# Performance work log

Hardware: AMD Instinct MI355X
Metric: run time of the kernel (lower is better)

The kernel has to match this reference:

```python
import jax, jax.numpy as jnp
import numpy as np

DIM = 384
HEADS = 8


def _dwconv3x3(x, w):
    # depthwise 3x3, groups = channels, padding=1 (SAME)
    return jax.lax.conv_general_dilated(
        x, w, window_strides=(1, 1), padding='SAME',
        feature_group_count=x.shape[1],
        dimension_numbers=('NCHW', 'OIHW', 'NCHW'))


def _conv1x1(x, w):
    return jax.lax.conv_general_dilated(
        x, w, window_strides=(1, 1), padding='SAME',
        dimension_numbers=('NCHW', 'OIHW', 'NCHW'))


def setup_inputs() -> dict:
    key = jax.random.key(0)
    ks = jax.random.split(key, 7)
    b, h, w = 2, 128, 128
    f = lambda k, s: jax.random.normal(k, s, dtype=jnp.float32)
    return {
        'k_fea': f(ks[0], (b, DIM, h, w)),
        'v_fea': f(ks[1], (b, DIM, h, w)),
        'q_fea': f(ks[2], (b, DIM, h, w)),
        'wq': f(ks[3], (DIM, 1, 3, 3)) * 0.1,
        'wk': f(ks[4], (DIM, 1, 3, 3)) * 0.1,
        'wv': f(ks[5], (DIM, 1, 3, 3)) * 0.1,
        'wproj': f(ks[6], (DIM, DIM, 1, 1)) * 0.05,
        'temperature': jnp.ones((HEADS, 1, 1), jnp.float32),
        'attn_w': jnp.full((4,), 0.2, jnp.float32),  # attn1..attn4 scalars
    }


def reference(k_fea, v_fea, q_fea, wq, wk, wv, wproj, temperature, attn_w):
    b, c, h, w = q_fea.shape
    q = _dwconv3x3(q_fea, wq)
    k = _dwconv3x3(k_fea, wk)
    v = _dwconv3x3(v_fea, wv)
    hw = h * w
    C = c // HEADS  # channels per head
    rs = lambda t: t.reshape(b, HEADS, C, hw)
    q, k, v = rs(q), rs(k), rs(v)
    # F.normalize(dim=-1): L2 normalize with eps clamp
    norm = lambda t: t / jnp.maximum(
        jnp.linalg.norm(t, axis=-1, keepdims=True), 1e-12)
    q, k = norm(q), norm(k)
    # channel-channel attention [b, heads, C, C]
    attn = jnp.einsum('bhcn,bhdn->bhcd', q, k) * temperature
    ar = jnp.arange(C)
    neg_inf = jnp.float32(-jnp.inf)
    ks_list = [C // 2, C * 2 // 3, C * 3 // 4, C * 4 // 5]
    out = jnp.zeros((b, HEADS, C, hw), attn.dtype)
    for i, topk in enumerate(ks_list):
        idx = jax.lax.top_k(attn, topk)[1]          # [b,h,C,topk]
        mask = (idx[..., None] == ar).any(axis=-2)  # [b,h,C,C] bool
        a = jax.nn.softmax(jnp.where(mask, attn, neg_inf), axis=-1)
        out = out + attn_w[i] * jnp.einsum('bhcd,bhdn->bhcn', a, v)
    out = out.reshape(b, c, h, w)
    return _conv1x1(out, wproj)
```

## Files before the change

kernel.cpp:

```cpp
#include <hip/hip_runtime.h>
#include <stdint.h>

#define NB 2
#define CH 384
#define NH 8
#define CPH 48
#define IMG 128
#define HW 16384

typedef float f32x4 __attribute__((ext_vector_type(4)));
typedef short bf16x8 __attribute__((ext_vector_type(8)));
typedef short short4v __attribute__((ext_vector_type(4)));

__device__ inline unsigned short f2bf(float f){
    unsigned u = __builtin_bit_cast(unsigned, f);
    u += 0x7FFFu + ((u >> 16) & 1u);
    return (unsigned short)(u >> 16);
}
__device__ inline float bf2f(unsigned short h){
    unsigned u = ((unsigned)h) << 16;
    return __builtin_bit_cast(float, u);
}

__global__ __launch_bounds__(256) void k_conv3(
    const float* __restrict__ qf, const float* __restrict__ kf,
    const float* __restrict__ vf,
    const float* __restrict__ wq, const float* __restrict__ wk,
    const float* __restrict__ wv,
    unsigned short* __restrict__ Qh, unsigned short* __restrict__ Ql,
    unsigned short* __restrict__ Kh, unsigned short* __restrict__ Kl,
    unsigned short* __restrict__ Vc, float* __restrict__ ssqg)
{
    const int p = blockIdx.x;
    const int tensor = p / 768;
    const int bc = p % 768;
    const int ch = bc % CH, b = bc / CH;

    const float* plane; const float* wp9;
    unsigned short *oh, *ol;
    if (tensor == 0) { plane = qf + (size_t)bc * HW; wp9 = wq + ch * 9;
                       oh = Qh + (size_t)bc * HW; ol = Ql + (size_t)bc * HW; }
    else if (tensor == 1) { plane = kf + (size_t)bc * HW; wp9 = wk + ch * 9;
                       oh = Kh + (size_t)bc * HW; ol = Kl + (size_t)bc * HW; }
    else             { plane = vf + (size_t)bc * HW; wp9 = wv + ch * 9;
                       oh = Vc + (size_t)bc * HW; ol = nullptr; }

    float w9[9];
#pragma unroll
    for (int i = 0; i < 9; ++i) w9[i] = wp9[i];

    const int t = threadIdx.x;
    const int wvid = t >> 6, lane = t & 63;
    const int rb = lane >> 5, cx = lane & 31;

    float ssqacc = 0.f;

    for (int pass = 0; pass < 16; ++pass) {
        const int y = wvid * 32 + pass * 2 + rb;
        float o0 = 0.f, o1 = 0.f, o2 = 0.f, o3 = 0.f;
#pragma unroll
        for (int dy = 0; dy < 3; ++dy) {
            const int yy = y + dy - 1;
            const float vm = (yy >= 0 && yy < IMG) ? 1.f : 0.f;
            const int yc = yy < 0 ? 0 : (yy > IMG - 1 ? IMG - 1 : yy);
            float4 r4 = *(const float4*)(plane + yc * IMG + 4 * cx);
            r4.x *= vm; r4.y *= vm; r4.z *= vm; r4.w *= vm;
            float lf = __shfl(r4.w, (lane + 63) & 63);
            if (cx == 0) lf = 0.f;
            float rt = __shfl(r4.x, (lane + 1) & 63);
            if (cx == 31) rt = 0.f;
            const float a0 = w9[dy * 3], a1 = w9[dy * 3 + 1], a2 = w9[dy * 3 + 2];
            o0 += a0 * lf   + a1 * r4.x + a2 * r4.y;
            o1 += a0 * r4.x + a1 * r4.y + a2 * r4.z;
            o2 += a0 * r4.y + a1 * r4.z + a2 * r4.w;
            o3 += a0 * r4.z + a1 * r4.w + a2 * rt;
        }
        const int xb = 4 * cx;
        if (tensor < 2) {
            ssqacc += o0 * o0 + o1 * o1 + o2 * o2 + o3 * o3;
            unsigned short h0 = f2bf(o0), h1 = f2bf(o1), h2 = f2bf(o2), h3 = f2bf(o3);
            short4v hv = {(short)h0, (short)h1, (short)h2, (short)h3};
            short4v lv = {(short)f2bf(o0 - bf2f(h0)), (short)f2bf(o1 - bf2f(h1)),
                          (short)f2bf(o2 - bf2f(h2)), (short)f2bf(o3 - bf2f(h3))};
            *(short4v*)(oh + y * IMG + xb) = hv;
            *(short4v*)(ol + y * IMG + xb) = lv;
        } else {
            short4v pv = {(short)f2bf(o0), (short)f2bf(o1), (short)f2bf(o2), (short)f2bf(o3)};
            *(short4v*)(oh + y * IMG + xb) = pv;
        }
    }

    if (tensor < 2) {
#pragma unroll
        for (int off = 32; off; off >>= 1) ssqacc += __shfl_xor(ssqacc, off);
        __shared__ float ssr[4];
        if (lane == 0) ssr[wvid] = ssqacc;
        __syncthreads();
        if (t == 0) {
            int h = ch / CPH, c = ch % CPH;
            ssqg[(b * NH + h) * 96 + tensor * 48 + c] = ssr[0] + ssr[1] + ssr[2] + ssr[3];
        }
    }
}

__global__ __launch_bounds__(256) void k_gram2(
    const unsigned short* __restrict__ Qh, const unsigned short* __restrict__ Ql,
    const unsigned short* __restrict__ Kh, const unsigned short* __restrict__ Kl,
    float* __restrict__ Sg)
{
    __shared__ float sred[4][2304];
    const int t = threadIdx.x;
    const int s = blockIdx.x, bh = blockIdx.y;
    const int wid = t >> 6, lane = t & 63, quad = lane >> 4, l15 = lane & 15;
    const size_t pbase = (size_t)((bh >> 3) * CH + (bh & 7) * CPH) * HW;

    f32x4 acc[3][3];
#pragma unroll
    for (int i = 0; i < 3; ++i)
#pragma unroll
        for (int j = 0; j < 3; ++j) acc[i][j] = (f32x4){0.f, 0.f, 0.f, 0.f};

    const int k0 = s * 512 + wid * 128;
#pragma unroll
    for (int ks = 0; ks < 4; ++ks) {
        const int px = k0 + ks * 32 + quad * 8;
        bf16x8 qh[3], ql_[3], kh[3], kl[3];
#pragma unroll
        for (int i = 0; i < 3; ++i) {
            size_t off = pbase + (size_t)(i * 16 + l15) * HW + px;
            qh[i]  = *(const bf16x8*)(Qh + off);
            ql_[i] = *(const bf16x8*)(Ql + off);
            kh[i]  = *(const bf16x8*)(Kh + off);
            kl[i]  = *(const bf16x8*)(Kl + off);
        }
#pragma unroll
        for (int ci = 0; ci < 3; ++ci)
#pragma unroll
            for (int di = 0; di < 3; ++di) {
                acc[ci][di] = __builtin_amdgcn_mfma_f32_16x16x32_bf16(qh[ci],  kh[di], acc[ci][di], 0, 0, 0);
                acc[ci][di] = __builtin_amdgcn_mfma_f32_16x16x32_bf16(qh[ci],  kl[di], acc[ci][di], 0, 0, 0);
                acc[ci][di] = __builtin_amdgcn_mfma_f32_16x16x32_bf16(ql_[ci], kh[di], acc[ci][di], 0, 0, 0);
            }
    }
#pragma unroll
    for (int ci = 0; ci < 3; ++ci)
#pragma unroll
        for (int di = 0; di < 3; ++di)
#pragma unroll
            for (int r = 0; r < 4; ++r)
                sred[wid][(ci * 16 + quad * 4 + r) * 48 + di * 16 + l15] = acc[ci][di][r];
    __syncthreads();
    float* Sbh = Sg + (size_t)bh * 2304;
#pragma unroll
    for (int i = 0; i < 9; ++i) {
        int e = t * 9 + i;
        atomicAdd(&Sbh[e], sred[0][e] + sred[1][e] + sred[2][e] + sred[3][e]);
    }
}

__global__ void k_attn(const float* __restrict__ Sg, const float* __restrict__ ssqg,
                       const float* __restrict__ temp, const float* __restrict__ aw,
                       float* __restrict__ Mg)
{
    const int t = threadIdx.x;
    const int r = blockIdx.x * 4 + (t >> 6);
    const int lane = t & 63;
    const int c = r % 48, h = (r / 48) % NH, b = r / (48 * NH);
    const float* Srow = Sg + ((size_t)(b * NH + h) * 48 + c) * 48;
    const float* sq = ssqg + (size_t)(b * NH + h) * 96;

    float v = -3.0e38f;
    if (lane < 48) {
        float nq = fmaxf(sqrtf(sq[c]), 1e-12f);
        float nk = fmaxf(sqrtf(sq[48 + lane]), 1e-12f);
        v = Srow[lane] / (nq * nk) * temp[h];
    }
    float m = v;
#pragma unroll
    for (int off = 32; off; off >>= 1) m = fmaxf(m, __shfl_xor(m, off));
    int rank = 0;
    for (int e = 0; e < 48; ++e) {
        float ve = __shfl(v, e);
        rank += ((ve > v) || (ve == v && e < lane)) ? 1 : 0;
    }
    float ed = (lane < 48) ? __expf(v - m) : 0.f;
    const int K4[4] = {24, 32, 36, 38};
    float f = 0.f;
#pragma unroll
    for (int i = 0; i < 4; ++i) {
        float x = (rank < K4[i]) ? ed : 0.f;
#pragma unroll
        for (int off = 32; off; off >>= 1) x += __shfl_xor(x, off);
        if (rank < K4[i]) f += aw[i] / x;
    }
    if (lane < 48) Mg[((size_t)(b * NH + h) * 48 + c) * 48 + lane] = ed * f;
}

__global__ void k_w2(const float* __restrict__ wproj, const float* __restrict__ Mg,
                     unsigned short* __restrict__ W2)
{
    int idx = blockIdx.x * 256 + threadIdx.x;
    int gd = idx % 384; int co = (idx / 384) % 384; int b = idx / (384 * 384);
    int h = gd / 48, d = gd % 48;
    const float* wp = wproj + (size_t)co * 384 + h * 48;
    const float* Mp = Mg + (size_t)(b * NH + h) * 2304 + d;
    float s = 0.f;
#pragma unroll
    for (int cc = 0; cc < 48; ++cc) s += wp[cc] * Mp[cc * 48];
    W2[idx] = f2bf(s);
}

__global__ __launch_bounds__(256) void k_trans(const unsigned short* __restrict__ Vc,
                                               unsigned short* __restrict__ Vct)
{
    __shared__ unsigned short S[64][66];
    const int nt = blockIdx.x, ct = blockIdx.y, b = blockIdx.z;
    const int t = threadIdx.x, r = t >> 2, seg = t & 3;
    const unsigned short* src = Vc + (size_t)(b * CH + ct * 64 + r) * HW + nt * 64 + seg * 16;
    *(bf16x8*)&S[r][seg * 16]     = *(const bf16x8*)src;
    *(bf16x8*)&S[r][seg * 16 + 8] = *(const bf16x8*)(src + 8);
    __syncthreads();
    unsigned short tmp[16];
#pragma unroll
    for (int i = 0; i < 16; ++i) tmp[i] = S[seg * 16 + i][r];
    unsigned short* dst = Vct + ((size_t)b * HW + nt * 64 + r) * CH + ct * 64 + seg * 16;
    *(bf16x8*)dst       = *(const bf16x8*)&tmp[0];
    *(bf16x8*)(dst + 8) = *(const bf16x8*)&tmp[8];
}

__global__ __launch_bounds__(256) void k_gemm2(const unsigned short* __restrict__ W2,
        const unsigned short* __restrict__ Vct, float* __restrict__ out)
{
    const int t = threadIdx.x;
    const int y = blockIdx.x, mt = blockIdx.y, b = blockIdx.z;
    const int wid = t >> 6, lane = t & 63, quad = lane >> 4, l15 = lane & 15;
    const int wm = wid >> 1, wn = wid & 1;

    f32x4 acc[4][4];
#pragma unroll
    for (int i = 0; i < 4; ++i)
#pragma unroll
        for (int j = 0; j < 4; ++j) acc[i][j] = (f32x4){0.f, 0.f, 0.f, 0.f};

    const unsigned short* Ab[4];
    const unsigned short* Bb[4];
#pragma unroll
    for (int i = 0; i < 4; ++i) {
        Ab[i] = W2 + (size_t)(b * CH + mt * 128 + wm * 64 + i * 16 + l15) * CH + quad * 8;
        Bb[i] = Vct + ((size_t)b * HW + y * IMG + wn * 64 + i * 16 + l15) * CH + quad * 8;
    }

    for (int kt = 0; kt < 12; ++kt) {
        const int K0 = kt * 32;
        bf16x8 af[4], bfr[4];
#pragma unroll
        for (int i = 0; i < 4; ++i) af[i]  = *(const bf16x8*)(Ab[i] + K0);
#pragma unroll
        for (int i = 0; i < 4; ++i) bfr[i] = *(const bf16x8*)(Bb[i] + K0);
#pragma unroll
        for (int mi = 0; mi < 4; ++mi)
#pragma unroll
            for (int ni = 0; ni < 4; ++ni)
                acc[mi][ni] = __builtin_amdgcn_mfma_f32_16x16x32_bf16(af[mi], bfr[ni], acc[mi][ni], 0, 0, 0);
    }
#pragma unroll
    for (int mi = 0; mi < 4; ++mi)
#pragma unroll
        for (int ni = 0; ni < 4; ++ni)
#pragma unroll
            for (int r = 0; r < 4; ++r) {
                int co = mt * 128 + wm * 64 + mi * 16 + quad * 4 + r;
                int n  = y * IMG + wn * 64 + ni * 16 + l15;
                out[(size_t)(b * CH + co) * HW + n] = acc[mi][ni][r];
            }
}

extern "C" void kernel_launch(void* const* d_in, const int* in_sizes, int n_in,
                              void* d_out, int out_size, void* d_ws, size_t ws_size,
                              hipStream_t stream)
{
    const float* k_fea = (const float*)d_in[0];
    const float* v_fea = (const float*)d_in[1];
    const float* q_fea = (const float*)d_in[2];
    const float* wq = (const float*)d_in[3];
    const float* wk = (const float*)d_in[4];
    const float* wv = (const float*)d_in[5];
    const float* wproj = (const float*)d_in[6];
    const float* temp = (const float*)d_in[7];
    const float* aw = (const float*)d_in[8];
    float* out = (float*)d_out;

    char* ws = (char*)d_ws;
    float* Sg   = (float*)ws;
    float* ssqg = (float*)(ws + 147456);
    float* Mg   = (float*)(ws + 153600);
    unsigned short* W2 = (unsigned short*)(ws + 301056);

    const size_t PLANE_BYTES = (size_t)NB * CH * HW * 2;
    unsigned short* Qh  = (unsigned short*)(ws + 890880);
    unsigned short* Ql  = (unsigned short*)(ws + 890880 + PLANE_BYTES);
    unsigned short* Kh  = (unsigned short*)(ws + 890880 + 2 * PLANE_BYTES);
    unsigned short* Kl  = (unsigned short*)(ws + 890880 + 3 * PLANE_BYTES);
    unsigned short* Vc  = (unsigned short*)(ws + 890880 + 4 * PLANE_BYTES);
    unsigned short* Vct = (unsigned short*)(ws + 890880 + 5 * PLANE_BYTES);

    hipMemsetAsync(Sg, 0, 147456, stream);
    k_conv3<<<2304, 256, 0, stream>>>(q_fea, k_fea, v_fea, wq, wk, wv,
                                      Qh, Ql, Kh, Kl, Vc, ssqg);
    k_gram2<<<dim3(32, 16), 256, 0, stream>>>(Qh, Ql, Kh, Kl, Sg);
    k_attn<<<192, 256, 0, stream>>>(Sg, ssqg, temp, aw, Mg);
    k_w2<<<1152, 256, 0, stream>>>(wproj, Mg, W2);
    k_trans<<<dim3(256, 6, 2), 256, 0, stream>>>(Vc, Vct);
    k_gemm2<<<dim3(128, 3, 2), 256, 0, stream>>>(W2, Vct, out);
}
```

Measured before the change: 319.2 us.

## Fuse Q/K depthwise conv into Gram kernel, drop bf16 hi/lo intermediates

The Q and K 3x3 depthwise convolutions are now computed inside the Gram-matrix MFMA kernel, with each wave producing one image row and splitting values into bf16 hi/lo in registers. This removes writing and re-reading four bf16 plane buffers (Qh, Ql, Kh, Kl). Per-channel squared norms are accumulated with atomics, and the memset is widened to cover them. V keeps a separate conv kernel. The trade-off is that the Gram kernel now does scalar conv math and unaligned neighbour loads, with more register pressure, across only 512 blocks.

```diff
diff --git a/kernel.cpp b/kernel.cpp
--- a/kernel.cpp
+++ b/kernel.cpp
@@ -22,28 +22,146 @@
     return __builtin_bit_cast(float, u);
 }
 
-__global__ __launch_bounds__(256) void k_conv3(
+__device__ __forceinline__ void conv8(const float* __restrict__ pl,
+                                      const float* w9, int x, int y, float* o)
+{
+#pragma unroll
+    for (int j = 0; j < 8; ++j) o[j] = 0.f;
+#pragma unroll
+    for (int dy = 0; dy < 3; ++dy) {
+        const int yy = y + dy - 1;
+        const float vm = (yy >= 0 && yy < IMG) ? 1.f : 0.f;
+        const int yc = yy < 0 ? 0 : (yy > IMG - 1 ? IMG - 1 : yy);
+        const float* row = pl + yc * IMG;
+        float4 A  = *(const float4*)(row + x);
+        float4 Bv = *(const float4*)(row + x + 4);
+        float lf = (x > 0)       ? row[x - 1] * vm : 0.f;
+        float rt = (x < IMG - 8) ? row[x + 8] * vm : 0.f;
+        A.x *= vm; A.y *= vm; A.z *= vm; A.w *= vm;
+        Bv.x *= vm; Bv.y *= vm; Bv.z *= vm; Bv.w *= vm;
+        const float a0 = w9[dy * 3], a1 = w9[dy * 3 + 1], a2 = w9[dy * 3 + 2];
+        o[0] += a0 * lf   + a1 * A.x  + a2 * A.y;
+        o[1] += a0 * A.x  + a1 * A.y  + a2 * A.z;
+        o[2] += a0 * A.y  + a1 * A.z  + a2 * A.w;
+        o[3] += a0 * A.z  + a1 * A.w  + a2 * Bv.x;
+        o[4] += a0 * A.w  + a1 * Bv.x + a2 * Bv.y;
+        o[5] += a0 * Bv.x + a1 * Bv.y + a2 * Bv.z;
+        o[6] += a0 * Bv.y + a1 * Bv.z + a2 * Bv.w;
+        o[7] += a0 * Bv.z + a1 * Bv.w + a2 * rt;
+    }
+}
+
+__device__ __forceinline__ void packhl(const float* o, bf16x8& hi, bf16x8& lo,
+                                       float& sq)
+{
+#pragma unroll
+    for (int j = 0; j < 8; ++j) {
+        sq += o[j] * o[j];
+        unsigned short hh = f2bf(o[j]);
+        hi[j] = (short)hh;
+        lo[j] = (short)f2bf(o[j] - bf2f(hh));
+    }
+}
+
+__global__ __launch_bounds__(256) void k_gramf(
     const float* __restrict__ qf, const float* __restrict__ kf,
-    const float* __restrict__ vf,
     const float* __restrict__ wq, const float* __restrict__ wk,
-    const float* __restrict__ wv,
-    unsigned short* __restrict__ Qh, unsigned short* __restrict__ Ql,
-    unsigned short* __restrict__ Kh, unsigned short* __restrict__ Kl,
-    unsigned short* __restrict__ Vc, float* __restrict__ ssqg)
-{
-    const int p = blockIdx.x;
-    const int tensor = p / 768;
-    const int bc = p % 768;
-    const int ch = bc % CH, b = bc / CH;
-
-    const float* plane; const float* wp9;
-    unsigned short *oh, *ol;
-    if (tensor == 0) { plane = qf + (size_t)bc * HW; wp9 = wq + ch * 9;
-                       oh = Qh + (size_t)bc * HW; ol = Ql + (size_t)bc * HW; }
-    else if (tensor == 1) { plane = kf + (size_t)bc * HW; wp9 = wk + ch * 9;
-                       oh = Kh + (size_t)bc * HW; ol = Kl + (size_t)bc * HW; }
-    else             { plane = vf + (size_t)bc * HW; wp9 = wv + ch * 9;
-                       oh = Vc + (size_t)bc * HW; ol = nullptr; }
+    float* __restrict__ Sg, float* __restrict__ ssqg)
+{
+    __shared__ float sred[4][2304];
+    __shared__ float ssr[4][96];
+    const int t = threadIdx.x;
+    const int s = blockIdx.x, bh = blockIdx.y;
+    const int wid = t >> 6, lane = t & 63, quad = lane >> 4, l15 = lane & 15;
+    const int b = bh >> 3, h = bh & 7;
+    const int y = s * 4 + wid;
+
+    const float* qpl[3];
+    const float* kpl[3];
+    float wqr[3][9], wkr[3][9];
+#pragma unroll
+    for (int i = 0; i < 3; ++i) {
+        const int c = h * CPH + i * 16 + l15;
+        qpl[i] = qf + (size_t)(b * CH + c) * HW;
+        kpl[i] = kf + (size_t)(b * CH + c) * HW;
+#pragma unroll
+        for (int j = 0; j < 9; ++j) {
+            wqr[i][j] = wq[c * 9 + j];
+            wkr[i][j] = wk[c * 9 + j];
+        }
+    }
+
+    f32x4 acc[3][3];
+#pragma unroll
+    for (int i = 0; i < 3; ++i)
+#pragma unroll
+        for (int j = 0; j < 3; ++j) acc[i][j] = (f32x4){0.f, 0.f, 0.f, 0.f};
+    float sqq[3] = {0.f, 0.f, 0.f}, sqk[3] = {0.f, 0.f, 0.f};
+
+    for (int ks = 0; ks < 4; ++ks) {
+        const int x = ks * 32 + quad * 8;
+        bf16x8 qh[3], ql_[3], kh[3], kl[3];
+#pragma unroll
+        for (int i = 0; i < 3; ++i) {
+            float o[8];
+            conv8(qpl[i], wqr[i], x, y, o);
+            packhl(o, qh[i], ql_[i], sqq[i]);
+            conv8(kpl[i], wkr[i], x, y, o);
+            packhl(o, kh[i], kl[i], sqk[i]);
+        }
+#pragma unroll
+        for (int ci = 0; ci < 3; ++ci)
+#pragma unroll
+            for (int di = 0; di < 3; ++di) {
+                acc[ci][di] = __builtin_amdgcn_mfma_f32_16x16x32_bf16(qh[ci],  kh[di], acc[ci][di], 0, 0, 0);
+                acc[ci][di] = __builtin_amdgcn_mfma_f32_16x16x32_bf16(qh[ci],  kl[di], acc[ci][di], 0, 0, 0);
+                acc[ci][di] = __builtin_amdgcn_mfma_f32_16x16x32_bf16(ql_[ci], kh[di], acc[ci][di], 0, 0, 0);
+            }
+    }
+
+#pragma unroll
+    for (int i = 0; i < 3; ++i) {
+#pragma unroll
+        for (int off = 16; off <= 32; off <<= 1) {
+            sqq[i] += __shfl_xor(sqq[i], off);
+            sqk[i] += __shfl_xor(sqk[i], off);
+        }
+        if (lane < 16) {
+            ssr[wid][i * 16 + l15]      = sqq[i];
+            ssr[wid][48 + i * 16 + l15] = sqk[i];
+        }
+    }
+
+#pragma unroll
+    for (int ci = 0; ci < 3; ++ci)
+#pragma unroll
+        for (int di = 0; di < 3; ++di)
+#pragma unroll
+            for (int r = 0; r < 4; ++r)
+                sred[wid][(ci * 16 + quad * 4 + r) * 48 + di * 16 + l15] = acc[ci][di][r];
+    __syncthreads();
+
+    if (t < 96)
+        atomicAdd(&ssqg[(size_t)bh * 96 + t],
+                  ssr[0][t] + ssr[1][t] + ssr[2][t] + ssr[3][t]);
+
+    float* Sbh = Sg + (size_t)bh * 2304;
+#pragma unroll
+    for (int i = 0; i < 9; ++i) {
+        int e = t * 9 + i;
+        atomicAdd(&Sbh[e], sred[0][e] + sred[1][e] + sred[2][e] + sred[3][e]);
+    }
+}
+
+__global__ __launch_bounds__(256) void k_conv3v(
+    const float* __restrict__ vf, const float* __restrict__ wv,
+    unsigned short* __restrict__ Vc)
+{
+    const int bc = blockIdx.x;
+    const int ch = bc % CH;
+    const float* plane = vf + (size_t)bc * HW;
+    const float* wp9 = wv + ch * 9;
+    unsigned short* oh = Vc + (size_t)bc * HW;
 
     float w9[9];
 #pragma unroll
@@ -52,8 +170,6 @@
     const int t = threadIdx.x;
     const int wvid = t >> 6, lane = t & 63;
     const int rb = lane >> 5, cx = lane & 31;
-
-    float ssqacc = 0.f;
 
     for (int pass = 0; pass < 16; ++pass) {
         const int y = wvid * 32 + pass * 2 + rb;
@@ -75,86 +191,8 @@
             o2 += a0 * r4.y + a1 * r4.z + a2 * r4.w;
             o3 += a0 * r4.z + a1 * r4.w + a2 * rt;
         }
-        const int xb = 4 * cx;
-        if (tensor < 2) {
-            ssqacc += o0 * o0 + o1 * o1 + o2 * o2 + o3 * o3;
-            unsigned short h0 = f2bf(o0), h1 = f2bf(o1), h2 = f2bf(o2), h3 = f2bf(o3);
-            short4v hv = {(short)h0, (short)h1, (short)h2, (short)h3};
-            short4v lv = {(short)f2bf(o0 - bf2f(h0)), (short)f2bf(o1 - bf2f(h1)),
-                          (short)f2bf(o2 - bf2f(h2)), (short)f2bf(o3 - bf2f(h3))};
-            *(short4v*)(oh + y * IMG + xb) = hv;
-            *(short4v*)(ol + y * IMG + xb) = lv;
-        } else {
-            short4v pv = {(short)f2bf(o0), (short)f2bf(o1), (short)f2bf(o2), (short)f2bf(o3)};
-            *(short4v*)(oh + y * IMG + xb) = pv;
-        }
-    }
-
-    if (tensor < 2) {
-#pragma unroll
-        for (int off = 32; off; off >>= 1) ssqacc += __shfl_xor(ssqacc, off);
-        __shared__ float ssr[4];
-        if (lane == 0) ssr[wvid] = ssqacc;
-        __syncthreads();
-        if (t == 0) {
-            int h = ch / CPH, c = ch % CPH;
-            ssqg[(b * NH + h) * 96 + tensor * 48 + c] = ssr[0] + ssr[1] + ssr[2] + ssr[3];
-        }
-    }
-}
-
-__global__ __launch_bounds__(256) void k_gram2(
-    const unsigned short* __restrict__ Qh, const unsigned short* __restrict__ Ql,
-    const unsigned short* __restrict__ Kh, const unsigned short* __restrict__ Kl,
-    float* __restrict__ Sg)
-{
-    __shared__ float sred[4][2304];
-    const int t = threadIdx.x;
-    const int s = blockIdx.x, bh = blockIdx.y;
-    const int wid = t >> 6, lane = t & 63, quad = lane >> 4, l15 = lane & 15;
-    const size_t pbase = (size_t)((bh >> 3) * CH + (bh & 7) * CPH) * HW;
-
-    f32x4 acc[3][3];
-#pragma unroll
-    for (int i = 0; i < 3; ++i)
-#pragma unroll
-        for (int j = 0; j < 3; ++j) acc[i][j] = (f32x4){0.f, 0.f, 0.f, 0.f};
-
-    const int k0 = s * 512 + wid * 128;
-#pragma unroll
-    for (int ks = 0; ks < 4; ++ks) {
-        const int px = k0 + ks * 32 + quad * 8;
-        bf16x8 qh[3], ql_[3], kh[3], kl[3];
-#pragma unroll
-        for (int i = 0; i < 3; ++i) {
-            size_t off = pbase + (size_t)(i * 16 + l15) * HW + px;
-            qh[i]  = *(const bf16x8*)(Qh + off);
-            ql_[i] = *(const bf16x8*)(Ql + off);
-            kh[i]  = *(const bf16x8*)(Kh + off);
-            kl[i]  = *(const bf16x8*)(Kl + off);
-        }
-#pragma unroll
-        for (int ci = 0; ci < 3; ++ci)
-#pragma unroll
-            for (int di = 0; di < 3; ++di) {
-                acc[ci][di] = __builtin_amdgcn_mfma_f32_16x16x32_bf16(qh[ci],  kh[di], acc[ci][di], 0, 0, 0);
-                acc[ci][di] = __builtin_amdgcn_mfma_f32_16x16x32_bf16(qh[ci],  kl[di], acc[ci][di], 0, 0, 0);
-                acc[ci][di] = __builtin_amdgcn_mfma_f32_16x16x32_bf16(ql_[ci], kh[di], acc[ci][di], 0, 0, 0);
-            }
-    }
-#pragma unroll
-    for (int ci = 0; ci < 3; ++ci)
-#pragma unroll
-        for (int di = 0; di < 3; ++di)
-#pragma unroll
-            for (int r = 0; r < 4; ++r)
-                sred[wid][(ci * 16 + quad * 4 + r) * 48 + di * 16 + l15] = acc[ci][di][r];
-    __syncthreads();
-    float* Sbh = Sg + (size_t)bh * 2304;
-#pragma unroll
-    for (int i = 0; i < 9; ++i) {
-        int e = t * 9 + i;
-        atomicAdd(&Sbh[e], sred[0][e] + sred[1][e] + sred[2][e] + sred[3][e]);
+        short4v pv = {(short)f2bf(o0), (short)f2bf(o1), (short)f2bf(o2), (short)f2bf(o3)};
+        *(short4v*)(oh + y * IMG + 4 * cx) = pv;
     }
 }
 
@@ -297,17 +335,12 @@
     unsigned short* W2 = (unsigned short*)(ws + 301056);
 
     const size_t PLANE_BYTES = (size_t)NB * CH * HW * 2;
-    unsigned short* Qh  = (unsigned short*)(ws + 890880);
-    unsigned short* Ql  = (unsigned short*)(ws + 890880 + PLANE_BYTES);
-    unsigned short* Kh  = (unsigned short*)(ws + 890880 + 2 * PLANE_BYTES);
-    unsigned short* Kl  = (unsigned short*)(ws + 890880 + 3 * PLANE_BYTES);
-    unsigned short* Vc  = (unsigned short*)(ws + 890880 + 4 * PLANE_BYTES);
-    unsigned short* Vct = (unsigned short*)(ws + 890880 + 5 * PLANE_BYTES);
-
-    hipMemsetAsync(Sg, 0, 147456, stream);
-    k_conv3<<<2304, 256, 0, stream>>>(q_fea, k_fea, v_fea, wq, wk, wv,
-                                      Qh, Ql, Kh, Kl, Vc, ssqg);
-    k_gram2<<<dim3(32, 16), 256, 0, stream>>>(Qh, Ql, Kh, Kl, Sg);
+    unsigned short* Vc  = (unsigned short*)(ws + 890880);
+    unsigned short* Vct = (unsigned short*)(ws + 890880 + PLANE_BYTES);
+
+    hipMemsetAsync(Sg, 0, 153600, stream);
+    k_conv3v<<<768, 256, 0, stream>>>(v_fea, wv, Vc);
+    k_gramf<<<dim3(32, 16), 256, 0, stream>>>(q_fea, k_fea, wq, wk, Sg, ssqg);
     k_attn<<<192, 256, 0, stream>>>(Sg, ssqg, temp, aw, Mg);
     k_w2<<<1152, 256, 0, stream>>>(wproj, Mg, W2);
     k_trans<<<dim3(256, 6, 2), 256, 0, stream>>>(Vc, Vct);
```

Measured after the change: 378.6 us. 1.19x slower.
